# Kernel optimization log

Measured on AMD Instinct MI355X. Metric: run time of the kernel, lower is better.

Reference implementation:

```python
import jax, jax.numpy as jnp
import numpy as np

B, H, C = 131072, 16, 32        # batch, n_holidays, n_changepoints
HID, HP, SKU = 512, 512 // 16, 64  # hidden_dim, hidden per holiday, sku embed dim
TEMP = 0.7
TIME_MAX = 365.0
LN_EPS = 1e-3  # keras LayerNormalization default epsilon


def mish(x):
    return x * jnp.tanh(jax.nn.softplus(x))


def setup_inputs() -> dict:
    key = jax.random.key(0)
    ks = jax.random.split(key, 12)
    inputs = jax.random.uniform(ks[0], (B, H), dtype=jnp.float32) * TIME_MAX
    sku_embedding = jax.random.normal(ks[1], (B, SKU), dtype=jnp.float32)
    # per-holiday params, stacked over holiday axis
    deltas = jnp.full((H, C), TIME_MAX / C, dtype=jnp.float32)  # changepoint_deltas init
    ln_gamma = jnp.ones((H, C), dtype=jnp.float32)
    ln_beta = jnp.zeros((H, C), dtype=jnp.float32)
    attn_w = jax.random.normal(ks[2], (H,), dtype=jnp.float32) * 0.5  # Dense(1) on [...,1]
    Wh = jax.random.normal(ks[3], (H, C, HP), dtype=jnp.float32) * (1.0 / np.sqrt(C))
    Wah = jax.random.normal(ks[4], (HID, HID), dtype=jnp.float32) * (1.0 / np.sqrt(HID))
    Waa = jax.random.normal(ks[5], (HID, HID), dtype=jnp.float32) * (1.0 / np.sqrt(HID))
    Wb = jax.random.normal(ks[6], (SKU, HID), dtype=jnp.float32) * (1.0 / np.sqrt(SKU))
    Wa = jax.random.normal(ks[7], (SKU, HID), dtype=jnp.float32) * (1.0 / np.sqrt(SKU))
    Wo = jax.random.normal(ks[8], (HID, 1), dtype=jnp.float32)
    Wo = Wo / jnp.linalg.norm(Wo, axis=0, keepdims=True)  # UnitNorm(axis=0) constraint
    return {"inputs": inputs, "sku_embedding": sku_embedding, "deltas": deltas,
            "ln_gamma": ln_gamma, "ln_beta": ln_beta, "attn_w": attn_w, "Wh": Wh,
            "Wah": Wah, "Waa": Waa, "Wb": Wb, "Wa": Wa, "Wo": Wo}


def reference(inputs, sku_embedding, deltas, ln_gamma, ln_beta, attn_w, Wh, Wah, Waa, Wb, Wa, Wo):
    # ChangepointReLU (vectorised over holidays): softplus -> cumsum -> rescale to [0, 365]
    pd = jax.nn.softplus(deltas)                     # [H, C]
    cps = jnp.cumsum(pd, axis=-1)
    cps = cps / cps[:, -1:] * TIME_MAX               # time_min = 0
    feats = jax.nn.relu(inputs[:, :, None] - cps[None, :, :])  # [B, H, C]
    # per-holiday LayerNorm over changepoint axis
    mu = jnp.mean(feats, axis=-1, keepdims=True)
    var = jnp.mean((feats - mu) ** 2, axis=-1, keepdims=True)
    normed = (feats - mu) * jax.lax.rsqrt(var + LN_EPS) * ln_gamma[None] + ln_beta[None]
    # per-holiday attention: Dense(1,no bias) on [...,1] == scalar multiply per holiday
    logits = normed * attn_w[None, :, None]
    attn = jax.nn.softmax(logits / TEMP, axis=-1)    # n_changepoints > 1
    attended = normed * attn                          # [B, H, C]
    # per-holiday hidden Dense(HP, mish, no bias), then concat over holidays
    hid = mish(jnp.einsum('bhc,hcd->bhd', attended, Wh))  # [B, H, HP]
    aggregated = hid.reshape(hid.shape[0], H * HP)        # [B, HID]
    agg_hidden = mish(aggregated @ Wah)                   # [B, HID]
    agg_attn = jax.nn.softmax((agg_hidden @ Waa) / TEMP, axis=-1)
    final = agg_hidden * agg_attn                         # dropout inactive (inference)
    beta = jax.nn.sigmoid(sku_embedding @ Wb)
    alpha = sku_embedding @ Wa
    final = final * beta + alpha
    return final @ Wo                                     # [B, 1]
```

## Files before the change

kernel.cpp:

```cpp
#include <hip/hip_runtime.h>
#include <hip/hip_fp16.h>
#include <stdint.h>

#define B_TOT 131072
#define CHUNK 65536
#define NH 16
#define NC 32
#define HIDD 512

typedef unsigned short u16;
typedef unsigned int u32;
typedef __attribute__((ext_vector_type(8))) short short8;
typedef __attribute__((ext_vector_type(4))) float f32x4;
typedef __attribute__((ext_vector_type(4))) int i32x4;

#define GLLDS(g, l) __builtin_amdgcn_global_load_lds((const __attribute__((address_space(1))) unsigned int*)(g), (__attribute__((address_space(3))) unsigned int*)(l), 16, 0, 0)

__device__ __forceinline__ u16 f2bf(float x){
  unsigned u = __float_as_uint(x);
  u += 0x7fffu + ((u >> 16) & 1u);
  return (u16)(u >> 16);
}
__device__ __forceinline__ float bf2f(u16 b){ return __uint_as_float(((unsigned)b) << 16); }
__device__ __forceinline__ u16 f2h(float x){ __half h = __float2half(x); return *(u16*)&h; }
__device__ __forceinline__ float h2f(u16 b){ __half h; *(u16*)&h = b; return __half2float(h); }
__device__ __forceinline__ float mishf(float x){
  float e = __expf(fminf(x, 30.f));
  float u = 1.f + e;
  float u2 = u * u;
  return x * (u2 - 1.f) * __builtin_amdgcn_rcpf(u2 + 1.f);
}

__global__ void prep_small(const float* __restrict__ deltas, const float* __restrict__ Wa,
                           const float* __restrict__ Wo, float* __restrict__ cps, float* __restrict__ wWo)
{
  const int t = threadIdx.x;
  if (t < NH){
    float cum[NC];
    float run = 0.f;
#pragma unroll
    for (int c = 0; c < NC; c++){
      float d = deltas[t*NC + c];
      float sp = (d > 20.f) ? d : log1pf(__expf(d));
      run += sp; cum[c] = run;
    }
    float s = 365.0f / run;
#pragma unroll
    for (int c = 0; c < NC; c++) cps[t*NC + c] = cum[c] * s;
  } else if (t >= 64 && t < 128){
    const int k = t - 64;
    float s = 0.f;
    for (int n = 0; n < HIDD; n++) s += Wa[k*HIDD + n] * Wo[n];
    wWo[k] = s;
  }
}

__global__ void prep_convert(const float* __restrict__ Wah, const float* __restrict__ Waa,
                             const float* __restrict__ Wb, const float* __restrict__ Wh,
                             u16* __restrict__ WahT, u16* __restrict__ WaaT,
                             u16* __restrict__ WbT, u16* __restrict__ WhT)
{
  int i = blockIdx.x * 256 + threadIdx.x;
  if (i < 262144){ int n = i >> 9, k = i & 511; WahT[i] = f2bf(Wah[k*512 + n]); return; }
  i -= 262144;
  if (i < 262144){ int n = i >> 9, k = i & 511; WaaT[i] = f2bf(Waa[k*512 + n]); return; }
  i -= 262144;
  if (i < 32768){ int n = i >> 6, k = i & 63; WbT[i] = f2bf(Wb[k*512 + n]); return; }
  i -= 32768;
  if (i < 16384){ int h = i >> 10, r = i & 1023, d = r >> 5, c = r & 31;
                  WhT[i] = f2bf(Wh[h*1024 + c*32 + d]); return; }
}

__global__ __launch_bounds__(256) void stage1_kernel(
    const float* __restrict__ inputs, const float* __restrict__ sku,
    const float* __restrict__ ln_g, const float* __restrict__ ln_b,
    const float* __restrict__ attnw, const float* __restrict__ cps,
    const float* __restrict__ wWo, const u16* __restrict__ WhT,
    u16* __restrict__ agg, u16* __restrict__ skub, float* __restrict__ skd)
{
  __shared__ __align__(16) float in_l[256];
  __shared__ __align__(16) float cps_l[512];
  __shared__ __align__(16) float gam_l[512];
  __shared__ __align__(16) float bet_l[512];
  __shared__ float aw_l[16];
  __shared__ __align__(16) u16 at_l[16*16*32];
  __shared__ __align__(16) u16 ot_l[16*512];

  const int t = threadIdx.x;
  const int ln = t & 63;
  const long bb = (long)blockIdx.x * 64;

  cps_l[t] = cps[t];       cps_l[t+256] = cps[t+256];
  gam_l[t] = ln_g[t];      gam_l[t+256] = ln_g[t+256];
  bet_l[t] = ln_b[t];      bet_l[t+256] = ln_b[t+256];
  if (t < 16) aw_l[t] = attnw[t];
  in_l[t] = inputs[bb*16 + t];

#pragma unroll
  for (int it = 0; it < 4; it++){
    const long bs = bb + it*16;
    const f32x4 sv = *(const f32x4*)&sku[bs*64 + t*4];
    unsigned lo = (unsigned)f2bf(sv.x) | ((unsigned)f2bf(sv.y) << 16);
    unsigned hi = (unsigned)f2bf(sv.z) | ((unsigned)f2bf(sv.w) << 16);
    unsigned long long v = (unsigned long long)lo | ((unsigned long long)hi << 32);
    *(unsigned long long*)&skub[bs*64 + t*4] = v;
    const f32x4 wv4 = *(const f32x4*)&wWo[(ln & 15)*4];
    float pd = sv.x*wv4.x + sv.y*wv4.y + sv.z*wv4.z + sv.w*wv4.w;
#pragma unroll
    for (int s = 1; s < 16; s <<= 1) pd += __shfl_xor(pd, s);
    if ((ln & 15) == 0) skd[bs + (t >> 4)] = pd;
  }

  const int h = t >> 4, bi = t & 15;
  const int wv = t >> 6;
  const int lrow = ln & 15, lq = ln >> 4;

  short8 wf0[4], wf1[4];
#pragma unroll
  for (int q = 0; q < 4; q++){
    const int hh = wv*4 + q;
    wf0[q] = *(const short8*)&WhT[hh*1024 + lrow*32 + lq*8];
    wf1[q] = *(const short8*)&WhT[hh*1024 + (16 + lrow)*32 + lq*8];
  }
  __syncthreads();

#pragma unroll 1
  for (int it = 0; it < 4; it++){
    const float x = in_l[bi*16 + h];
    const float awv = aw_l[h] * (1.0f/0.7f);
    float nrm[NC];
    float s1 = 0.f;
#pragma unroll
    for (int c = 0; c < NC; c++){ float f = fmaxf(x - cps_l[h*NC + c], 0.f); nrm[c] = f; s1 += f; }
    const float mu = s1 * (1.f/NC);
    float s2 = 0.f;
#pragma unroll
    for (int c = 0; c < NC; c++){ float d = nrm[c] - mu; s2 += d*d; }
    const float rs = rsqrtf(s2 * (1.f/NC) + 1e-3f);
    float lmax = -1e30f;
#pragma unroll
    for (int c = 0; c < NC; c++){
      float nv = (nrm[c] - mu) * rs * gam_l[h*NC + c] + bet_l[h*NC + c];
      nrm[c] = nv;
      lmax = fmaxf(lmax, nv * awv);
    }
    float ps = 0.f;
#pragma unroll
    for (int c = 0; c < NC; c++) ps += __expf(nrm[c]*awv - lmax);
    const float invs = __builtin_amdgcn_rcpf(ps);
#pragma unroll
    for (int c = 0; c < NC; c += 2){
      const float p0 = __expf(nrm[c]*awv - lmax) * invs;
      const float p1 = __expf(nrm[c+1]*awv - lmax) * invs;
      unsigned pk = (unsigned)f2bf(nrm[c]*p0) | ((unsigned)f2bf(nrm[c+1]*p1) << 16);
      *(unsigned*)&at_l[h*512 + bi*32 + c] = pk;
    }
    __syncthreads();

    if (it < 3) in_l[t] = inputs[(bb + (it+1)*16)*16 + t];

#pragma unroll
    for (int q = 0; q < 4; q++){
      const int hh = wv*4 + q;
      short8 af = *(const short8*)&at_l[hh*512 + lrow*32 + lq*8];
      f32x4 acc0 = {0.f,0.f,0.f,0.f}, acc1 = {0.f,0.f,0.f,0.f};
      acc0 = __builtin_amdgcn_mfma_f32_16x16x32_bf16(af, wf0[q], acc0, 0, 0, 0);
      acc1 = __builtin_amdgcn_mfma_f32_16x16x32_bf16(af, wf1[q], acc1, 0, 0, 0);
#pragma unroll
      for (int r = 0; r < 4; r++){
        const int br = lq*4 + r;
        ot_l[br*512 + hh*32 + lrow]      = f2bf(mishf(acc0[r]));
        ot_l[br*512 + hh*32 + 16 + lrow] = f2bf(mishf(acc1[r]));
      }
    }
    __syncthreads();

    {
      const int row = t >> 4, c16 = t & 15;
      const i32x4* src = (const i32x4*)&ot_l[row*512 + c16*32];
      i32x4* dst = (i32x4*)&agg[(bb + it*16 + row)*512 + c16*32];
#pragma unroll
      for (int j = 0; j < 4; j++) dst[j] = src[j];
    }
    __syncthreads();
  }
}

#define PHASE(KH, MH) do { \
  const int buf_ = kt & 1; \
  const int abase_ = buf_*16384 + (KH)*8192; \
  const int bbase_ = 32768 + buf_*16384 + (KH)*8192; \
  short8 a_[4], b_[4]; \
  _Pragma("unroll") \
  for (int i = 0; i < 4; i++){ \
    const int row_ = wm*128 + (MH)*64 + i*16 + lrow; \
    a_[i] = *(const short8*)&smem[abase_ + row_*32 + (lq ^ ((row_ >> 1) & 3))*8]; \
    const int nrow_ = wn*64 + i*16 + lrow; \
    b_[i] = *(const short8*)&smem[bbase_ + nrow_*32 + (lq ^ ((nrow_ >> 1) & 3))*8]; \
  } \
  __builtin_amdgcn_s_setprio(1); \
  _Pragma("unroll") \
  for (int i = 0; i < 4; i++) \
    _Pragma("unroll") \
    for (int j = 0; j < 4; j++) \
      acc[(MH)*4 + i][j] = __builtin_amdgcn_mfma_f32_16x16x32_bf16(a_[i], b_[j], acc[(MH)*4 + i][j], 0, 0, 0); \
  __builtin_amdgcn_s_setprio(0); \
} while(0)

__global__ __launch_bounds__(512, 1) void gemm1(
    const u16* __restrict__ A, const u16* __restrict__ Bt, u16* __restrict__ aggh)
{
  __shared__ __align__(16) u16 smem[65536];
  const int t = threadIdx.x, wid = t >> 6, ln = t & 63;
  const int lrow = ln & 15, lq = ln >> 4;
  const int wm = wid >> 2, wn = wid & 3;
  const int g = blockIdx.x;
  const long m0 = (long)(g >> 1) * 256;
  const int n0 = (g & 1) * 256;

  auto stageA = [&](int kt_, int kh_){
#pragma unroll
    for (int l = 0; l < 2; l++){
      const int slot = t + l*512;
      const int row = slot >> 2, kc = slot & 3;
      const int kcl = kc ^ ((row >> 1) & 3);
      GLLDS(&A[(m0 + row)*512 + kt_*64 + kh_*32 + kcl*8],
            &smem[(kt_ & 1)*16384 + kh_*8192 + slot*8]);
    }
  };
  auto stageB = [&](int kt_, int kh_){
#pragma unroll
    for (int l = 0; l < 2; l++){
      const int slot = t + l*512;
      const int row = slot >> 2, kc = slot & 3;
      const int kcl = kc ^ ((row >> 1) & 3);
      GLLDS(&Bt[(n0 + row)*512 + kt_*64 + kh_*32 + kcl*8],
            &smem[32768 + (kt_ & 1)*16384 + kh_*8192 + slot*8]);
    }
  };

  f32x4 acc[8][4] = {};
  stageA(0, 0); stageB(0, 0); stageA(0, 1); stageB(0, 1); stageA(1, 0); stageB(1, 0);

#pragma unroll 1
  for (int kt = 0; kt < 8; kt++){
    if (kt < 7) asm volatile("s_waitcnt vmcnt(8)" ::: "memory");
    else        asm volatile("s_waitcnt vmcnt(4)" ::: "memory");
    __builtin_amdgcn_s_barrier();
    if (kt + 1 < 8) stageA(kt + 1, 1);
    PHASE(0, 0);
    __builtin_amdgcn_s_barrier();
    if (kt + 1 < 8) stageB(kt + 1, 1);
    PHASE(0, 1);
    if (kt < 7) asm volatile("s_waitcnt vmcnt(8)" ::: "memory");
    else        asm volatile("s_waitcnt vmcnt(0)" ::: "memory");
    __builtin_amdgcn_s_barrier();
    if (kt + 2 < 8) stageA(kt + 2, 0);
    PHASE(1, 0);
    __builtin_amdgcn_s_barrier();
    if (kt + 2 < 8) stageB(kt + 2, 0);
    PHASE(1, 1);
  }

  __syncthreads();
  const int TP = 264;
#pragma unroll 1
  for (int h = 0; h < 2; h++){
    if (wm == h){
#pragma unroll
      for (int mh = 0; mh < 2; mh++)
#pragma unroll
        for (int i = 0; i < 4; i++)
#pragma unroll
          for (int j = 0; j < 4; j++)
#pragma unroll
            for (int r = 0; r < 4; r++){
              const int row = mh*64 + i*16 + lq*4 + r;
              smem[row*TP + wn*64 + j*16 + lrow] = f2bf(mishf(acc[mh*4 + i][j][r]));
            }
    }
    __syncthreads();
#pragma unroll
    for (int it = 0; it < 8; it++){
      const int idx = it*512 + t;
      const int row = idx >> 5, ch = idx & 31;
      const i32x4 v = *(const i32x4*)&smem[row*TP + ch*8];
      *(i32x4*)&aggh[(m0 + h*128 + row)*512 + n0 + ch*8] = v;
    }
    __syncthreads();
  }
}
#undef PHASE

__global__ __launch_bounds__(256, 3) void mega2f(
    const u16* __restrict__ A, const u16* __restrict__ Bt,
    const u16* __restrict__ skub, const u16* __restrict__ WbT,
    const float* __restrict__ Wo, float* __restrict__ part)
{
  __shared__ __align__(16) u16 smem[24576];
  const int t = threadIdx.x, wv = t >> 6, ln = t & 63;
  const int g = blockIdx.x;
  const int m_idx = (g & 7) + ((g >> 5) << 3);
  const int n_idx = (g >> 3) & 3;
  const long m0 = (long)m_idx * 128;
  const int n0 = n_idx * 128;
  const int lrow = ln & 15, lq = ln >> 4;
  const int wm = wv >> 1, wn = wv & 1;
  const float inv_t = 1.0f / 0.7f;

  u32 bwp[4][4][2];
  {
    auto stage3 = [&](int buf, int kt){
#pragma unroll
      for (int p = 0; p < 2; p++){
        const int chunk = p*256 + wv*64 + ln;
        const int mm = chunk >> 2, kc = chunk & 3;
        const int kcl = kc ^ ((mm >> 1) & 3);
        GLLDS(&skub[(m0 + mm)*64 + kt + kcl*8], &smem[buf*4096 + (p*256 + wv*64)*8]);
        GLLDS(&WbT[(n0 + mm)*64 + kt + kcl*8],  &smem[8192 + buf*4096 + (p*256 + wv*64)*8]);
      }
    };
    f32x4 acc3[4][4] = {};
    stage3(0, 0); stage3(1, 32);
    asm volatile("s_waitcnt vmcnt(0)" ::: "memory");
    __builtin_amdgcn_s_barrier();
#pragma unroll
    for (int ks3 = 0; ks3 < 2; ks3++){
      short8 a3[4], b3[4];
#pragma unroll
      for (int i = 0; i < 4; i++){
        const int ra = wm*64 + i*16 + lrow;
        const int rb = wn*64 + i*16 + lrow;
        const int lqa = lq ^ ((ra >> 1) & 3);
        const int lqb = lq ^ ((rb >> 1) & 3);
        a3[i] = *(const short8*)&smem[ks3*4096 + ra*32 + lqa*8];
        b3[i] = *(const short8*)&smem[8192 + ks3*4096 + rb*32 + lqb*8];
      }
#pragma unroll
      for (int i = 0; i < 4; i++)
#pragma unroll
        for (int j = 0; j < 4; j++)
          acc3[i][j] = __builtin_amdgcn_mfma_f32_16x16x32_bf16(a3[i], b3[j], acc3[i][j], 0, 0, 0);
    }
#pragma unroll
    for (int j = 0; j < 4; j++){
      const float wo = Wo[n0 + wn*64 + j*16 + lrow];
#pragma unroll
      for (int i = 0; i < 4; i++)
#pragma unroll
        for (int rp = 0; rp < 2; rp++){
          const float s0 = wo * __builtin_amdgcn_rcpf(1.f + __expf(-acc3[i][j][2*rp]));
          const float s1 = wo * __builtin_amdgcn_rcpf(1.f + __expf(-acc3[i][j][2*rp+1]));
          bwp[i][j][rp] = (u32)f2h(s0) | ((u32)f2h(s1) << 16);
        }
    }
  }
  __syncthreads();

  auto stage = [&](int buf, int kt){
#pragma unroll
    for (int p = 0; p < 2; p++){
      const int chunk = p*256 + wv*64 + ln;
      const int mm = chunk >> 2, kc = chunk & 3;
      const int kcl = kc ^ ((mm >> 1) & 3);
      GLLDS(&A[(m0 + mm)*512 + kt + kcl*8],  &smem[buf*4096 + (p*256 + wv*64)*8]);
      GLLDS(&Bt[(n0 + mm)*512 + kt + kcl*8], &smem[12288 + buf*4096 + (p*256 + wv*64)*8]);
    }
  };

  f32x4 acc[4][4] = {};
  stage(0, 0); stage(1, 32);
#pragma unroll 1
  for (int ks = 0; ks < 16; ks++){
    const int cur = ks % 3;
    if (ks < 15) asm volatile("s_waitcnt vmcnt(4)" ::: "memory");
    else         asm volatile("s_waitcnt vmcnt(0)" ::: "memory");
    __builtin_amdgcn_s_barrier();
    if (ks + 2 < 16) stage((ks + 2) % 3, (ks + 2)*32);
    short8 a[4], b[4];
#pragma unroll
    for (int i = 0; i < 4; i++){
      const int ra = wm*64 + i*16 + lrow;
      const int rb = wn*64 + i*16 + lrow;
      const int lqa = lq ^ ((ra >> 1) & 3);
      const int lqb = lq ^ ((rb >> 1) & 3);
      a[i] = *(const short8*)&smem[cur*4096 + ra*32 + lqa*8];
      b[i] = *(const short8*)&smem[12288 + cur*4096 + rb*32 + lqb*8];
    }
#pragma unroll
    for (int i = 0; i < 4; i++)
#pragma unroll
      for (int j = 0; j < 4; j++)
        acc[i][j] = __builtin_amdgcn_mfma_f32_16x16x32_bf16(a[i], b[j], acc[i][j], 0, 0, 0);
  }

  __syncthreads();
  float* mloc = (float*)smem;
  float* sloc = mloc + 256;
  float* tloc = sloc + 256;

#pragma unroll
  for (int i = 0; i < 4; i++){
#pragma unroll
    for (int r = 0; r < 4; r++){
      float tm = acc[i][0][r];
#pragma unroll
      for (int j = 1; j < 4; j++) tm = fmaxf(tm, acc[i][j][r]);
#pragma unroll
      for (int s = 1; s < 16; s <<= 1) tm = fmaxf(tm, __shfl_xor(tm, s));
      const int rowL = wm*64 + i*16 + lq*4 + r;
      float sp = 0.f, tp = 0.f;
#pragma unroll
      for (int j = 0; j < 4; j++){
        const long gi = (m0 + rowL)*512 + n0 + wn*64 + j*16 + lrow;
        const float e = __expf((acc[i][j][r] - tm) * inv_t);
        const u16 bh = (u16)(bwp[i][j][r >> 1] >> ((r & 1)*16));
        sp += e; tp += e * bf2f(A[gi]) * h2f(bh);
      }
#pragma unroll
      for (int s = 1; s < 16; s <<= 1){ sp += __shfl_xor(sp, s); tp += __shfl_xor(tp, s); }
      if (lrow == 0){
        mloc[rowL*2 + wn] = tm; sloc[rowL*2 + wn] = sp; tloc[rowL*2 + wn] = tp;
      }
    }
  }
  __syncthreads();
  if (t < 128){
    const float ma = mloc[t*2], mb = mloc[t*2 + 1];
    const float M = fmaxf(ma, mb);
    const float wa = __expf((ma - M) * inv_t), wb = __expf((mb - M) * inv_t);
    const float S = sloc[t*2]*wa + sloc[t*2 + 1]*wb;
    const float T = tloc[t*2]*wa + tloc[t*2 + 1]*wb;
    float* pm = part + (size_t)n_idx*3*CHUNK;
    pm[m0 + t]           = M;
    pm[CHUNK + m0 + t]   = S;
    pm[2*CHUNK + m0 + t] = T;
  }
}

__global__ __launch_bounds__(256) void combine_kernel(
    const float* __restrict__ part, const float* __restrict__ skd, float* __restrict__ outp)
{
  const int row = blockIdx.x*256 + threadIdx.x;
  const float inv_t = 1.0f / 0.7f;
  float M = -1e30f;
#pragma unroll
  for (int nt = 0; nt < 4; nt++) M = fmaxf(M, part[(size_t)nt*3*CHUNK + row]);
  float S = 0.f, T = 0.f;
#pragma unroll
  for (int nt = 0; nt < 4; nt++){
    const float w = __expf((part[(size_t)nt*3*CHUNK + row] - M) * inv_t);
    S += part[(size_t)nt*3*CHUNK + CHUNK + row] * w;
    T += part[(size_t)nt*3*CHUNK + 2*CHUNK + row] * w;
  }
  outp[row] = T / S + skd[row];
}

__global__ void ws_too_small(float* o, float v){ o[(long)blockIdx.x*256 + threadIdx.x] = v; }

extern "C" void kernel_launch(void* const* d_in, const int* in_sizes, int n_in,
                              void* d_out, int out_size, void* d_ws, size_t ws_size,
                              hipStream_t stream)
{
  const float* inputs = (const float*)d_in[0];
  const float* sku    = (const float*)d_in[1];
  const float* deltas = (const float*)d_in[2];
  const float* ln_g   = (const float*)d_in[3];
  const float* ln_b   = (const float*)d_in[4];
  const float* attnw  = (const float*)d_in[5];
  const float* Wh     = (const float*)d_in[6];
  const float* Wah    = (const float*)d_in[7];
  const float* Waa    = (const float*)d_in[8];
  const float* Wb     = (const float*)d_in[9];
  const float* Wa     = (const float*)d_in[10];
  const float* Wo     = (const float*)d_in[11];
  float* outp = (float*)d_out;

  const size_t OFF_CPS  = 0;
  const size_t OFF_WWO  = 2048;
  const size_t OFF_WAHT = 4096;
  const size_t OFF_WAAT = OFF_WAHT + 524288;
  const size_t OFF_WBT  = OFF_WAAT + 524288;
  const size_t OFF_WHT  = OFF_WBT  + 65536;
  const size_t OFF_SKUB = OFF_WHT  + 32768;
  const size_t OFF_SKD  = OFF_SKUB + (size_t)CHUNK*64*2;
  const size_t OFF_AGG  = OFF_SKD  + (size_t)CHUNK*4;
  const size_t OFF_AGH  = OFF_AGG  + (size_t)CHUNK*512*2;
  const size_t OFF_PART = OFF_AGH  + (size_t)CHUNK*512*2;
  const size_t NEED     = OFF_PART + (size_t)4*3*CHUNK*4;

  if (ws_size < NEED){
    hipLaunchKernelGGL(ws_too_small, dim3(B_TOT/256), dim3(256), 0, stream,
                       outp, -(float)(ws_size >> 20));
    return;
  }

  char* ws = (char*)d_ws;
  float* cps  = (float*)(ws + OFF_CPS);
  float* wWo  = (float*)(ws + OFF_WWO);
  u16* WahT   = (u16*)(ws + OFF_WAHT);
  u16* WaaT   = (u16*)(ws + OFF_WAAT);
  u16* WbT    = (u16*)(ws + OFF_WBT);
  u16* WhT    = (u16*)(ws + OFF_WHT);
  u16* skub   = (u16*)(ws + OFF_SKUB);
  float* skd  = (float*)(ws + OFF_SKD);
  u16* agg    = (u16*)(ws + OFF_AGG);
  u16* aggh   = (u16*)(ws + OFF_AGH);
  float* part = (float*)(ws + OFF_PART);

  hipLaunchKernelGGL(prep_small, dim3(1), dim3(128), 0, stream, deltas, Wa, Wo, cps, wWo);
  hipLaunchKernelGGL(prep_convert, dim3(2240), dim3(256), 0, stream,
                     Wah, Waa, Wb, Wh, WahT, WaaT, WbT, WhT);

  for (int ch = 0; ch < B_TOT / CHUNK; ch++){
    const float* in_c  = inputs + (size_t)ch * CHUNK * 16;
    const float* sku_c = sku    + (size_t)ch * CHUNK * 64;
    float* out_c       = outp   + (size_t)ch * CHUNK;

    hipLaunchKernelGGL(stage1_kernel, dim3(CHUNK/64), dim3(256), 0, stream,
                       in_c, sku_c, ln_g, ln_b, attnw, cps, wWo, WhT, agg, skub, skd);
    hipLaunchKernelGGL(gemm1, dim3(CHUNK/256*2), dim3(512), 0, stream,
                       agg, WahT, aggh);
    hipLaunchKernelGGL(mega2f, dim3(CHUNK/128*4), dim3(256), 0, stream,
                       aggh, WaaT, skub, WbT, Wo, part);
    hipLaunchKernelGGL(combine_kernel, dim3(CHUNK/256), dim3(256), 0, stream,
                       part, skd, out_c);
  }
}
```

Measured before the change: 465.9 us.

## Enlarge mega2f tiles to 256x256, share pipelined k-loop, drop stage1 barriers

The second fused GEMM kernel moves from 128x128 tiles with 256 threads to 256x256 tiles with 512 threads. It reuses gemm1's double-buffered, phase-split k-loop through a shared macro, which halves the number of partial softmax slices the combine kernel has to merge. Stage1 remaps threads so each wave owns its own holidays and rows, which lets it drop the shared input staging and all per-iteration block barriers. Both GEMMs also get a grouped block ordering meant to improve L2 reuse. The cost is heavier register pressure at one block per CU, and stage1 now relies on wave-local ordering of LDS writes and reads.

```diff
diff --git a/kernel.cpp b/kernel.cpp
--- a/kernel.cpp
+++ b/kernel.cpp
@@ -78,7 +78,6 @@
     const float* __restrict__ wWo, const u16* __restrict__ WhT,
     u16* __restrict__ agg, u16* __restrict__ skub, float* __restrict__ skd)
 {
-  __shared__ __align__(16) float in_l[256];
   __shared__ __align__(16) float cps_l[512];
   __shared__ __align__(16) float gam_l[512];
   __shared__ __align__(16) float bet_l[512];
@@ -94,7 +93,6 @@
   gam_l[t] = ln_g[t];      gam_l[t+256] = ln_g[t+256];
   bet_l[t] = ln_b[t];      bet_l[t+256] = ln_b[t+256];
   if (t < 16) aw_l[t] = attnw[t];
-  in_l[t] = inputs[bb*16 + t];
 
 #pragma unroll
   for (int it = 0; it < 4; it++){
@@ -111,9 +109,10 @@
     if ((ln & 15) == 0) skd[bs + (t >> 4)] = pd;
   }
 
-  const int h = t >> 4, bi = t & 15;
   const int wv = t >> 6;
   const int lrow = ln & 15, lq = ln >> 4;
+  const int h = wv*4 + (ln >> 4);
+  const int bi = ln & 15;
 
   short8 wf0[4], wf1[4];
 #pragma unroll
@@ -124,10 +123,11 @@
   }
   __syncthreads();
 
+  const float awv = aw_l[h] * (1.0f/0.7f);
+
 #pragma unroll 1
   for (int it = 0; it < 4; it++){
-    const float x = in_l[bi*16 + h];
-    const float awv = aw_l[h] * (1.0f/0.7f);
+    const float x = inputs[(bb + it*16 + bi)*16 + h];
     float nrm[NC];
     float s1 = 0.f;
 #pragma unroll
@@ -155,9 +155,6 @@
       unsigned pk = (unsigned)f2bf(nrm[c]*p0) | ((unsigned)f2bf(nrm[c+1]*p1) << 16);
       *(unsigned*)&at_l[h*512 + bi*32 + c] = pk;
     }
-    __syncthreads();
-
-    if (it < 3) in_l[t] = inputs[(bb + (it+1)*16)*16 + t];
 
 #pragma unroll
     for (int q = 0; q < 4; q++){
@@ -173,16 +170,14 @@
         ot_l[br*512 + hh*32 + 16 + lrow] = f2bf(mishf(acc1[r]));
       }
     }
-    __syncthreads();
 
     {
-      const int row = t >> 4, c16 = t & 15;
-      const i32x4* src = (const i32x4*)&ot_l[row*512 + c16*32];
-      i32x4* dst = (i32x4*)&agg[(bb + it*16 + row)*512 + c16*32];
+      const int drow = ln >> 2, dsub = ln & 3;
+      const i32x4* src = (const i32x4*)&ot_l[drow*512 + wv*128 + dsub*32];
+      i32x4* dst = (i32x4*)&agg[(bb + it*16 + drow)*512 + wv*128 + dsub*32];
 #pragma unroll
       for (int j = 0; j < 4; j++) dst[j] = src[j];
     }
-    __syncthreads();
   }
 }
 
@@ -207,6 +202,48 @@
   __builtin_amdgcn_s_setprio(0); \
 } while(0)
 
+#define KLOOP(SRC_A, SRC_B) \
+  auto stageA = [&](int kt_, int kh_){ \
+    _Pragma("unroll") \
+    for (int l = 0; l < 2; l++){ \
+      const int slot = t + l*512; \
+      const int row = slot >> 2, kc = slot & 3; \
+      const int kcl = kc ^ ((row >> 1) & 3); \
+      GLLDS(&SRC_A[(m0 + row)*512 + kt_*64 + kh_*32 + kcl*8], \
+            &smem[(kt_ & 1)*16384 + kh_*8192 + slot*8]); \
+    } \
+  }; \
+  auto stageB = [&](int kt_, int kh_){ \
+    _Pragma("unroll") \
+    for (int l = 0; l < 2; l++){ \
+      const int slot = t + l*512; \
+      const int row = slot >> 2, kc = slot & 3; \
+      const int kcl = kc ^ ((row >> 1) & 3); \
+      GLLDS(&SRC_B[(n0 + row)*512 + kt_*64 + kh_*32 + kcl*8], \
+            &smem[32768 + (kt_ & 1)*16384 + kh_*8192 + slot*8]); \
+    } \
+  }; \
+  stageA(0, 0); stageB(0, 0); stageA(0, 1); stageB(0, 1); stageA(1, 0); stageB(1, 0); \
+  _Pragma("unroll 1") \
+  for (int kt = 0; kt < 8; kt++){ \
+    if (kt < 7) asm volatile("s_waitcnt vmcnt(8)" ::: "memory"); \
+    else        asm volatile("s_waitcnt vmcnt(4)" ::: "memory"); \
+    __builtin_amdgcn_s_barrier(); \
+    if (kt + 1 < 8) stageA(kt + 1, 1); \
+    PHASE(0, 0); \
+    __builtin_amdgcn_s_barrier(); \
+    if (kt + 1 < 8) stageB(kt + 1, 1); \
+    PHASE(0, 1); \
+    if (kt < 7) asm volatile("s_waitcnt vmcnt(8)" ::: "memory"); \
+    else        asm volatile("s_waitcnt vmcnt(0)" ::: "memory"); \
+    __builtin_amdgcn_s_barrier(); \
+    if (kt + 2 < 8) stageA(kt + 2, 0); \
+    PHASE(1, 0); \
+    __builtin_amdgcn_s_barrier(); \
+    if (kt + 2 < 8) stageB(kt + 2, 0); \
+    PHASE(1, 1); \
+  }
+
 __global__ __launch_bounds__(512, 1) void gemm1(
     const u16* __restrict__ A, const u16* __restrict__ Bt, u16* __restrict__ aggh)
 {
@@ -215,52 +252,12 @@
   const int lrow = ln & 15, lq = ln >> 4;
   const int wm = wid >> 2, wn = wid & 3;
   const int g = blockIdx.x;
-  const long m0 = (long)(g >> 1) * 256;
-  const int n0 = (g & 1) * 256;
-
-  auto stageA = [&](int kt_, int kh_){
-#pragma unroll
-    for (int l = 0; l < 2; l++){
-      const int slot = t + l*512;
-      const int row = slot >> 2, kc = slot & 3;
-      const int kcl = kc ^ ((row >> 1) & 3);
-      GLLDS(&A[(m0 + row)*512 + kt_*64 + kh_*32 + kcl*8],
-            &smem[(kt_ & 1)*16384 + kh_*8192 + slot*8]);
-    }
-  };
-  auto stageB = [&](int kt_, int kh_){
-#pragma unroll
-    for (int l = 0; l < 2; l++){
-      const int slot = t + l*512;
-      const int row = slot >> 2, kc = slot & 3;
-      const int kcl = kc ^ ((row >> 1) & 3);
-      GLLDS(&Bt[(n0 + row)*512 + kt_*64 + kh_*32 + kcl*8],
-            &smem[32768 + (kt_ & 1)*16384 + kh_*8192 + slot*8]);
-    }
-  };
+  const int m_idx = (g & 7) + ((g >> 4) << 3);
+  const long m0 = (long)m_idx * 256;
+  const int n0 = ((g >> 3) & 1) * 256;
 
   f32x4 acc[8][4] = {};
-  stageA(0, 0); stageB(0, 0); stageA(0, 1); stageB(0, 1); stageA(1, 0); stageB(1, 0);
-
-#pragma unroll 1
-  for (int kt = 0; kt < 8; kt++){
-    if (kt < 7) asm volatile("s_waitcnt vmcnt(8)" ::: "memory");
-    else        asm volatile("s_waitcnt vmcnt(4)" ::: "memory");
-    __builtin_amdgcn_s_barrier();
-    if (kt + 1 < 8) stageA(kt + 1, 1);
-    PHASE(0, 0);
-    __builtin_amdgcn_s_barrier();
-    if (kt + 1 < 8) stageB(kt + 1, 1);
-    PHASE(0, 1);
-    if (kt < 7) asm volatile("s_waitcnt vmcnt(8)" ::: "memory");
-    else        asm volatile("s_waitcnt vmcnt(0)" ::: "memory");
-    __builtin_amdgcn_s_barrier();
-    if (kt + 2 < 8) stageA(kt + 2, 0);
-    PHASE(1, 0);
-    __builtin_amdgcn_s_barrier();
-    if (kt + 2 < 8) stageB(kt + 2, 0);
-    PHASE(1, 1);
-  }
+  KLOOP(A, Bt)
 
   __syncthreads();
   const int TP = 264;
@@ -290,54 +287,54 @@
     __syncthreads();
   }
 }
-#undef PHASE
-
-__global__ __launch_bounds__(256, 3) void mega2f(
+
+__global__ __launch_bounds__(512, 1) void mega2f(
     const u16* __restrict__ A, const u16* __restrict__ Bt,
     const u16* __restrict__ skub, const u16* __restrict__ WbT,
     const float* __restrict__ Wo, float* __restrict__ part)
 {
-  __shared__ __align__(16) u16 smem[24576];
-  const int t = threadIdx.x, wv = t >> 6, ln = t & 63;
+  __shared__ __align__(16) u16 smem[65536];
+  const int t = threadIdx.x, wid = t >> 6, ln = t & 63;
+  const int lrow = ln & 15, lq = ln >> 4;
+  const int wm = wid >> 2, wn = wid & 3;
   const int g = blockIdx.x;
-  const int m_idx = (g & 7) + ((g >> 5) << 3);
-  const int n_idx = (g >> 3) & 3;
-  const long m0 = (long)m_idx * 128;
-  const int n0 = n_idx * 128;
-  const int lrow = ln & 15, lq = ln >> 4;
-  const int wm = wv >> 1, wn = wv & 1;
+  const int m_idx = (g & 7) + ((g >> 4) << 3);
+  const int n_idx = (g >> 3) & 1;
+  const long m0 = (long)m_idx * 256;
+  const int n0 = n_idx * 256;
   const float inv_t = 1.0f / 0.7f;
 
-  u32 bwp[4][4][2];
+  u32 bwp[8][4][2];
   {
-    auto stage3 = [&](int buf, int kt){
-#pragma unroll
-      for (int p = 0; p < 2; p++){
-        const int chunk = p*256 + wv*64 + ln;
-        const int mm = chunk >> 2, kc = chunk & 3;
-        const int kcl = kc ^ ((mm >> 1) & 3);
-        GLLDS(&skub[(m0 + mm)*64 + kt + kcl*8], &smem[buf*4096 + (p*256 + wv*64)*8]);
-        GLLDS(&WbT[(n0 + mm)*64 + kt + kcl*8],  &smem[8192 + buf*4096 + (p*256 + wv*64)*8]);
+    auto stage3 = [&](int kh){
+#pragma unroll
+      for (int l = 0; l < 2; l++){
+        const int slot = t + l*512;
+        const int row = slot >> 2, kc = slot & 3;
+        const int kcl = kc ^ ((row >> 1) & 3);
+        GLLDS(&skub[(m0 + row)*64 + kh*32 + kcl*8], &smem[kh*8192 + slot*8]);
+        GLLDS(&WbT[(n0 + row)*64 + kh*32 + kcl*8],  &smem[32768 + kh*8192 + slot*8]);
       }
     };
-    f32x4 acc3[4][4] = {};
-    stage3(0, 0); stage3(1, 32);
+    f32x4 acc3[8][4] = {};
+    stage3(0); stage3(1);
     asm volatile("s_waitcnt vmcnt(0)" ::: "memory");
     __builtin_amdgcn_s_barrier();
 #pragma unroll
-    for (int ks3 = 0; ks3 < 2; ks3++){
-      short8 a3[4], b3[4];
-#pragma unroll
-      for (int i = 0; i < 4; i++){
-        const int ra = wm*64 + i*16 + lrow;
-        const int rb = wn*64 + i*16 + lrow;
-        const int lqa = lq ^ ((ra >> 1) & 3);
-        const int lqb = lq ^ ((rb >> 1) & 3);
-        a3[i] = *(const short8*)&smem[ks3*4096 + ra*32 + lqa*8];
-        b3[i] = *(const short8*)&smem[8192 + ks3*4096 + rb*32 + lqb*8];
+    for (int kh = 0; kh < 2; kh++){
+      short8 a3[8], b3[4];
+#pragma unroll
+      for (int i = 0; i < 8; i++){
+        const int row = wm*128 + i*16 + lrow;
+        a3[i] = *(const short8*)&smem[kh*8192 + row*32 + (lq ^ ((row >> 1) & 3))*8];
       }
 #pragma unroll
-      for (int i = 0; i < 4; i++)
+      for (int j = 0; j < 4; j++){
+        const int nrow = wn*64 + j*16 + lrow;
+        b3[j] = *(const short8*)&smem[32768 + kh*8192 + nrow*32 + (lq ^ ((nrow >> 1) & 3))*8];
+      }
+#pragma unroll
+      for (int i = 0; i < 8; i++)
 #pragma unroll
         for (int j = 0; j < 4; j++)
           acc3[i][j] = __builtin_amdgcn_mfma_f32_16x16x32_bf16(a3[i], b3[j], acc3[i][j], 0, 0, 0);
@@ -346,7 +343,7 @@
     for (int j = 0; j < 4; j++){
       const float wo = Wo[n0 + wn*64 + j*16 + lrow];
 #pragma unroll
-      for (int i = 0; i < 4; i++)
+      for (int i = 0; i < 8; i++)
 #pragma unroll
         for (int rp = 0; rp < 2; rp++){
           const float s0 = wo * __builtin_amdgcn_rcpf(1.f + __expf(-acc3[i][j][2*rp]));
@@ -357,86 +354,61 @@
   }
   __syncthreads();
 
-  auto stage = [&](int buf, int kt){
-#pragma unroll
-    for (int p = 0; p < 2; p++){
-      const int chunk = p*256 + wv*64 + ln;
-      const int mm = chunk >> 2, kc = chunk & 3;
-      const int kcl = kc ^ ((mm >> 1) & 3);
-      GLLDS(&A[(m0 + mm)*512 + kt + kcl*8],  &smem[buf*4096 + (p*256 + wv*64)*8]);
-      GLLDS(&Bt[(n0 + mm)*512 + kt + kcl*8], &smem[12288 + buf*4096 + (p*256 + wv*64)*8]);
-    }
-  };
-
-  f32x4 acc[4][4] = {};
-  stage(0, 0); stage(1, 32);
-#pragma unroll 1
-  for (int ks = 0; ks < 16; ks++){
-    const int cur = ks % 3;
-    if (ks < 15) asm volatile("s_waitcnt vmcnt(4)" ::: "memory");
-    else         asm volatile("s_waitcnt vmcnt(0)" ::: "memory");
-    __builtin_amdgcn_s_barrier();
-    if (ks + 2 < 16) stage((ks + 2) % 3, (ks + 2)*32);
-    short8 a[4], b[4];
-#pragma unroll
-    for (int i = 0; i < 4; i++){
-      const int ra = wm*64 + i*16 + lrow;
-      const int rb = wn*64 + i*16 + lrow;
-      const int lqa = lq ^ ((ra >> 1) & 3);
-      const int lqb = lq ^ ((rb >> 1) & 3);
-      a[i] = *(const short8*)&smem[cur*4096 + ra*32 + lqa*8];
-      b[i] = *(const short8*)&smem[12288 + cur*4096 + rb*32 + lqb*8];
-    }
-#pragma unroll
-    for (int i = 0; i < 4; i++)
-#pragma unroll
-      for (int j = 0; j < 4; j++)
-        acc[i][j] = __builtin_amdgcn_mfma_f32_16x16x32_bf16(a[i], b[j], acc[i][j], 0, 0, 0);
-  }
+  f32x4 acc[8][4] = {};
+  KLOOP(A, Bt)
 
   __syncthreads();
   float* mloc = (float*)smem;
-  float* sloc = mloc + 256;
-  float* tloc = sloc + 256;
-
-#pragma unroll
-  for (int i = 0; i < 4; i++){
-#pragma unroll
-    for (int r = 0; r < 4; r++){
-      float tm = acc[i][0][r];
-#pragma unroll
-      for (int j = 1; j < 4; j++) tm = fmaxf(tm, acc[i][j][r]);
-#pragma unroll
-      for (int s = 1; s < 16; s <<= 1) tm = fmaxf(tm, __shfl_xor(tm, s));
-      const int rowL = wm*64 + i*16 + lq*4 + r;
-      float sp = 0.f, tp = 0.f;
-#pragma unroll
-      for (int j = 0; j < 4; j++){
-        const long gi = (m0 + rowL)*512 + n0 + wn*64 + j*16 + lrow;
-        const float e = __expf((acc[i][j][r] - tm) * inv_t);
-        const u16 bh = (u16)(bwp[i][j][r >> 1] >> ((r & 1)*16));
-        sp += e; tp += e * bf2f(A[gi]) * h2f(bh);
+  float* sloc = mloc + 1024;
+  float* tloc = sloc + 1024;
+
+#pragma unroll
+  for (int mh = 0; mh < 2; mh++)
+#pragma unroll
+    for (int i = 0; i < 4; i++)
+#pragma unroll
+      for (int r = 0; r < 4; r++){
+        const int ai = mh*4 + i;
+        float tm = acc[ai][0][r];
+#pragma unroll
+        for (int j = 1; j < 4; j++) tm = fmaxf(tm, acc[ai][j][r]);
+#pragma unroll
+        for (int s = 1; s < 16; s <<= 1) tm = fmaxf(tm, __shfl_xor(tm, s));
+        const int rowL = wm*128 + mh*64 + i*16 + lq*4 + r;
+        float sp = 0.f, tp = 0.f;
+#pragma unroll
+        for (int j = 0; j < 4; j++){
+          const long gi = (m0 + rowL)*512 + n0 + wn*64 + j*16 + lrow;
+          const float e = __expf((acc[ai][j][r] - tm) * inv_t);
+          const u16 bh = (u16)(bwp[ai][j][r >> 1] >> ((r & 1)*16));
+          sp += e; tp += e * bf2f(A[gi]) * h2f(bh);
+        }
+#pragma unroll
+        for (int s = 1; s < 16; s <<= 1){ sp += __shfl_xor(sp, s); tp += __shfl_xor(tp, s); }
+        if (lrow == 0){
+          mloc[rowL*4 + wn] = tm; sloc[rowL*4 + wn] = sp; tloc[rowL*4 + wn] = tp;
+        }
       }
-#pragma unroll
-      for (int s = 1; s < 16; s <<= 1){ sp += __shfl_xor(sp, s); tp += __shfl_xor(tp, s); }
-      if (lrow == 0){
-        mloc[rowL*2 + wn] = tm; sloc[rowL*2 + wn] = sp; tloc[rowL*2 + wn] = tp;
-      }
-    }
-  }
   __syncthreads();
-  if (t < 128){
-    const float ma = mloc[t*2], mb = mloc[t*2 + 1];
-    const float M = fmaxf(ma, mb);
-    const float wa = __expf((ma - M) * inv_t), wb = __expf((mb - M) * inv_t);
-    const float S = sloc[t*2]*wa + sloc[t*2 + 1]*wb;
-    const float T = tloc[t*2]*wa + tloc[t*2 + 1]*wb;
+  if (t < 256){
+    float M = mloc[t*4];
+#pragma unroll
+    for (int k = 1; k < 4; k++) M = fmaxf(M, mloc[t*4 + k]);
+    float S = 0.f, T = 0.f;
+#pragma unroll
+    for (int k = 0; k < 4; k++){
+      const float w = __expf((mloc[t*4 + k] - M) * inv_t);
+      S += sloc[t*4 + k] * w;
+      T += tloc[t*4 + k] * w;
+    }
     float* pm = part + (size_t)n_idx*3*CHUNK;
     pm[m0 + t]           = M;
     pm[CHUNK + m0 + t]   = S;
     pm[2*CHUNK + m0 + t] = T;
   }
 }
+#undef KLOOP
+#undef PHASE
 
 __global__ __launch_bounds__(256) void combine_kernel(
     const float* __restrict__ part, const float* __restrict__ skd, float* __restrict__ outp)
@@ -445,10 +417,10 @@
   const float inv_t = 1.0f / 0.7f;
   float M = -1e30f;
 #pragma unroll
-  for (int nt = 0; nt < 4; nt++) M = fmaxf(M, part[(size_t)nt*3*CHUNK + row]);
+  for (int nt = 0; nt < 2; nt++) M = fmaxf(M, part[(size_t)nt*3*CHUNK + row]);
   float S = 0.f, T = 0.f;
 #pragma unroll
-  for (int nt = 0; nt < 4; nt++){
+  for (int nt = 0; nt < 2; nt++){
     const float w = __expf((part[(size_t)nt*3*CHUNK + row] - M) * inv_t);
     S += part[(size_t)nt*3*CHUNK + CHUNK + row] * w;
     T += part[(size_t)nt*3*CHUNK + 2*CHUNK + row] * w;
@@ -521,7 +493,7 @@
                        in_c, sku_c, ln_g, ln_b, attnw, cps, wWo, WhT, agg, skub, skd);
     hipLaunchKernelGGL(gemm1, dim3(CHUNK/256*2), dim3(512), 0, stream,
                        agg, WahT, aggh);
-    hipLaunchKernelGGL(mega2f, dim3(CHUNK/128*4), dim3(256), 0, stream,
+    hipLaunchKernelGGL(mega2f, dim3(CHUNK/256*2), dim3(512), 0, stream,
                        aggh, WaaT, skub, WbT, Wo, part);
     hipLaunchKernelGGL(combine_kernel, dim3(CHUNK/256), dim3(256), 0, stream,
                        part, skd, out_c);
```

After: 497.6 us. 6.8% more time.
